# Kernel tuning notes

Measured on AMD Instinct MI355X. Metric: run time of the kernel, lower is better.

## Reference

```python
import jax, jax.numpy as jnp
import numpy as np

# Config matching init_kwargs: N=4 networks, dims 128 -> 1024 -> 1024 -> 512
A, B, D = 8, 2048, 128     # agents, batch, input size
N = 4                       # number of independent SePS networks
H1, H2, H3 = 1024, 1024, 512


def setup_inputs() -> dict:
    key = jax.random.key(0)
    ks = jax.random.split(key, 6)
    inputs = jax.random.normal(ks[0], (A, B, D), dtype=jnp.float32)  # stacked per-agent obs
    seps_indices = jax.random.randint(ks[1], (B, A), 0, N)           # cluster id per (sample, agent)
    scale = lambda k, shape, fan: jax.random.normal(k, shape, dtype=jnp.float32) * (1.0 / np.sqrt(fan))
    W0 = scale(ks[2], (N, D, H1), D);   b0 = jnp.zeros((N, H1), jnp.float32)
    W1 = scale(ks[3], (N, H1, H2), H1); b1 = jnp.zeros((N, H2), jnp.float32)
    W2 = scale(ks[4], (N, H2, H3), H2); b2 = jnp.zeros((N, H3), jnp.float32)
    return {"inputs": inputs, "seps_indices": seps_indices,
            "W0": W0, "b0": b0, "W1": W1, "b1": b1, "W2": W2, "b2": b2}


def reference(inputs, seps_indices, W0, b0, W1, b1, W2, b2):
    # Run every network densely on the full stacked input, as the torch module does.
    # inputs: [A, B, D]; W*: [N, in, out]
    h = jax.nn.relu(jnp.einsum('abd,ndh->nabh', inputs, W0) + b0[:, None, None, :])
    h = jax.nn.relu(jnp.einsum('nabh,nhk->nabk', h, W1) + b1[:, None, None, :])
    out_all = jnp.einsum('nabk,nko->nabo', h, W2) + b2[:, None, None, :]  # [N, A, B, H3]
    # Gather along the network axis per (agent, sample): seps_indices is [B, A]
    idx = seps_indices.T                              # [A, B]
    a = jnp.arange(inputs.shape[0])[:, None]          # [A, 1]
    b = jnp.arange(inputs.shape[1])[None, :]          # [1, B]
    return out_all[idx, a, b, :]                      # [A, B, H3] (stacked per-agent outputs)
```

## Files before the change

kernel.cpp:

```cpp
#include <hip/hip_runtime.h>
#include <hip/hip_bf16.h>

#define AG 8
#define BT 2048
#define RT (AG*BT)
#define NNET 4
#define D0 128
#define H1 1024
#define H2 1024
#define H3 512

typedef __attribute__((ext_vector_type(8))) short short8;
typedef __attribute__((ext_vector_type(4))) float f32x4;

__device__ __forceinline__ float bf2f(unsigned short u){
  return __uint_as_float(((unsigned int)u) << 16);
}
__device__ __forceinline__ unsigned short f2bf(float f){
  unsigned int x = __float_as_uint(f);
  x += 0x7fff + ((x >> 16) & 1);
  return (unsigned short)(x >> 16);
}

__device__ __forceinline__ void gload_lds16(const void* g, void* l){
  __builtin_amdgcn_global_load_lds(
      (const __attribute__((address_space(1))) unsigned int*)g,
      (__attribute__((address_space(3))) unsigned int*)l, 16, 0, 0);
}

__device__ __forceinline__ int bucket_off(const int* counts, int n){
  int s = 0;
  #pragma unroll
  for (int i = 0; i < NNET-1; i++) if (i < n) s += counts[i];
  return s;
}

__global__ void k_init(int* counts){
  if (threadIdx.x < NNET) counts[threadIdx.x] = 0;
}

__global__ __launch_bounds__(256) void k_compact(const int* __restrict__ seps,
                          int* __restrict__ counts, int* __restrict__ rowlist){
  __shared__ int lcount[NNET];
  __shared__ int lbase[NNET];
  int t = blockIdx.x * 256 + threadIdx.x;
  if (threadIdx.x < NNET) lcount[threadIdx.x] = 0;
  __syncthreads();
  int a = t >> 11, b = t & (BT-1);
  int n = seps[b*AG + a];
  int lrank = atomicAdd(&lcount[n], 1);
  __syncthreads();
  if (threadIdx.x < NNET)
    lbase[threadIdx.x] = atomicAdd(&counts[threadIdx.x], lcount[threadIdx.x]);
  __syncthreads();
  rowlist[n*RT + lbase[n] + lrank] = t;
}

template<int K, int NOUT>
__global__ __launch_bounds__(256) void k_transpose(const float* __restrict__ W,
                                                   unsigned short* __restrict__ WT){
  __shared__ float tile[32][33];
  int n = blockIdx.z;
  int k0 = blockIdx.x*32, o0 = blockIdx.y*32;
  const float* Wn = W + (size_t)n*K*NOUT;
  unsigned short* WTn = WT + (size_t)n*NOUT*K;
  int tx = threadIdx.x & 31, ty0 = threadIdx.x >> 5;
  #pragma unroll
  for (int r = 0; r < 32; r += 8)
    tile[ty0 + r][tx] = Wn[(size_t)(k0 + ty0 + r)*NOUT + o0 + tx];
  __syncthreads();
  #pragma unroll
  for (int r = 0; r < 32; r += 8)
    WTn[(size_t)(o0 + ty0 + r)*K + k0 + tx] = f2bf(tile[tx][ty0 + r]);
}

__global__ __launch_bounds__(256) void k_gather0(const float* __restrict__ X,
                          const int* __restrict__ counts,
                          const int* __restrict__ rowlist, unsigned short* __restrict__ X0h){
  int n = blockIdx.y;
  int cnt = counts[n];
  int i = blockIdx.x*16 + (threadIdx.x >> 4);
  if (i >= cnt) return;
  int off = bucket_off(counts, n);
  int orig = rowlist[n*RT + i];
  int c = (threadIdx.x & 15) * 8;
  const float* src = X + (size_t)orig*D0 + c;
  float4 v0 = *(const float4*)src, v1 = *(const float4*)(src+4);
  ushort4 u0, u1;
  u0.x=f2bf(v0.x); u0.y=f2bf(v0.y); u0.z=f2bf(v0.z); u0.w=f2bf(v0.w);
  u1.x=f2bf(v1.x); u1.y=f2bf(v1.y); u1.z=f2bf(v1.z); u1.w=f2bf(v1.w);
  unsigned short* dst = X0h + (size_t)(off + i)*D0 + c;
  *(ushort4*)dst = u0; *(ushort4*)(dst+4) = u1;
}

template<int K, int NOUT, int RELU, int SCATTER>
__global__ __launch_bounds__(256) void k_mlp(
    const unsigned short* __restrict__ X,
    const unsigned short* __restrict__ WT,
    const float* __restrict__ Bias,
    const int* __restrict__ counts,
    const int* __restrict__ rowlist,
    unsigned short* __restrict__ Yh,
    float* __restrict__ Yf)
{
  const int n = blockIdx.z;
  const int cnt = counts[n];
  const int i0 = blockIdx.x * 128;
  if (i0 >= cnt) return;
  const int off = bucket_off(counts, n);
  const int bn = blockIdx.y * 128;

  __shared__ __align__(16) unsigned short As[2][128*32];
  __shared__ __align__(16) unsigned short Bs[2][128*32];
  __shared__ int rs[128];

  const int t = threadIdx.x, lane = t & 63, wave = t >> 6;
  const int wm = wave >> 1, wn = wave & 1;
  const int lr = lane & 15, g = lane >> 4;

  if (SCATTER && t < 128) rs[t] = rowlist[n*RT + min(i0 + t, cnt-1)];

  const unsigned short* pA[2]; const unsigned short* pB[2];
  unsigned int ldsoff[2];
  const unsigned short* WTn = WT + (size_t)n * NOUT * K;
  #pragma unroll
  for (int j = 0; j < 2; j++){
    int r  = (j*4 + wave)*16 + (lane >> 2);
    int ps = lane & 3;
    int ls = ps ^ ((r >> 1) & 3);
    int rA = min(i0 + r, cnt-1);
    pA[j] = X   + (size_t)(off + rA)*K + ls*8;
    pB[j] = WTn + (size_t)(bn  + r )*K + ls*8;
    ldsoff[j] = (unsigned)(j*4 + wave) * 512;
  }

  int aoff[4], boff[4];
  #pragma unroll
  for (int i = 0; i < 4; i++){
    int ra = wm*64 + i*16 + lr;
    aoff[i] = ra*32 + (g ^ ((ra>>1)&3))*8;
    int rb = wn*64 + i*16 + lr;
    boff[i] = rb*32 + (g ^ ((rb>>1)&3))*8;
  }

  #pragma unroll
  for (int j = 0; j < 2; j++){
    gload_lds16(pA[j], &As[0][ldsoff[j]]);
    gload_lds16(pB[j], &Bs[0][ldsoff[j]]);
    pA[j] += 32; pB[j] += 32;
  }
  __syncthreads();

  f32x4 acc[4][4] = {};
  int cur = 0;
  for (int k0 = 0; k0 < K; k0 += 32){
    if (k0 + 32 < K){
      #pragma unroll
      for (int j = 0; j < 2; j++){
        gload_lds16(pA[j], &As[cur^1][ldsoff[j]]);
        gload_lds16(pB[j], &Bs[cur^1][ldsoff[j]]);
        pA[j] += 32; pB[j] += 32;
      }
    }
    short8 av[4], bv[4];
    #pragma unroll
    for (int i = 0; i < 4; i++) av[i] = *(const short8*)&As[cur][aoff[i]];
    #pragma unroll
    for (int i = 0; i < 4; i++) bv[i] = *(const short8*)&Bs[cur][boff[i]];
    __builtin_amdgcn_s_setprio(1);
    #pragma unroll
    for (int mi = 0; mi < 4; mi++)
      #pragma unroll
      for (int ni = 0; ni < 4; ni++)
        acc[mi][ni] = __builtin_amdgcn_mfma_f32_16x16x32_bf16(bv[ni], av[mi], acc[mi][ni], 0, 0, 0);
    __builtin_amdgcn_s_setprio(0);
    __syncthreads();
    cur ^= 1;
  }

  f32x4 bias4[4];
  #pragma unroll
  for (int ni = 0; ni < 4; ni++)
    bias4[ni] = *(const f32x4*)&Bias[n*NOUT + bn + wn*64 + ni*16 + g*4];

  #pragma unroll
  for (int mi = 0; mi < 4; mi++){
    int rloc = wm*64 + mi*16 + lr;
    int grow = i0 + rloc;
    if (grow < cnt){
      #pragma unroll
      for (int ni = 0; ni < 4; ni++){
        float o[4];
        #pragma unroll
        for (int i = 0; i < 4; i++){
          float v = acc[mi][ni][i] + bias4[ni][i];
          if (RELU) v = fmaxf(v, 0.f);
          o[i] = v;
        }
        int cb = bn + wn*64 + ni*16 + (g<<2);
        if (SCATTER){
          *(float4*)&Yf[(size_t)rs[rloc]*NOUT + cb] = make_float4(o[0],o[1],o[2],o[3]);
        } else {
          ushort4 u;
          u.x=f2bf(o[0]); u.y=f2bf(o[1]); u.z=f2bf(o[2]); u.w=f2bf(o[3]);
          *(ushort4*)&Yh[(size_t)(off + grow)*NOUT + cb] = u;
        }
      }
    }
  }
}

extern "C" void kernel_launch(void* const* d_in, const int* in_sizes, int n_in,
                              void* d_out, int out_size, void* d_ws, size_t ws_size,
                              hipStream_t stream) {
  const float* inputs = (const float*)d_in[0];
  const int*   seps   = (const int*)  d_in[1];
  const float* W0     = (const float*)d_in[2];
  const float* b0     = (const float*)d_in[3];
  const float* W1     = (const float*)d_in[4];
  const float* b1     = (const float*)d_in[5];
  const float* W2     = (const float*)d_in[6];
  const float* b2     = (const float*)d_in[7];
  float* out = (float*)d_out;

  char* ws = (char*)d_ws;
  int* counts  = (int*)ws;
  int* rowlist = (int*)(ws + 4096);
  const size_t MB = 1u << 20;
  unsigned short* WT0 = (unsigned short*)(ws + 1*MB);
  unsigned short* WT1 = (unsigned short*)(ws + 2*MB);
  unsigned short* WT2 = (unsigned short*)(ws + 10*MB);
  unsigned short* h1  = (unsigned short*)(ws + 14*MB);
  unsigned short* h2  = (unsigned short*)(ws + 46*MB);
  unsigned short* X0h = (unsigned short*)(ws + 46*MB);

  k_init   <<<1, 64, 0, stream>>>(counts);
  k_compact<<<RT/256, 256, 0, stream>>>(seps, counts, rowlist);

  k_transpose<D0, H1><<<dim3(D0/32, H1/32, NNET), 256, 0, stream>>>(W0, WT0);
  k_transpose<H1, H2><<<dim3(H1/32, H2/32, NNET), 256, 0, stream>>>(W1, WT1);
  k_transpose<H2, H3><<<dim3(H2/32, H3/32, NNET), 256, 0, stream>>>(W2, WT2);
  k_gather0<<<dim3(RT/16, NNET), 256, 0, stream>>>(inputs, counts, rowlist, X0h);

  k_mlp<D0, H1, 1, 0><<<dim3(RT/128, H1/128, NNET), 256, 0, stream>>>(
      X0h, WT0, b0, counts, rowlist, h1, nullptr);
  k_mlp<H1, H2, 1, 0><<<dim3(RT/128, H2/128, NNET), 256, 0, stream>>>(
      h1, WT1, b1, counts, rowlist, h2, nullptr);
  k_mlp<H2, H3, 0, 1><<<dim3(RT/128, H3/128, NNET), 256, 0, stream>>>(
      h2, WT2, b2, counts, rowlist, nullptr, out);
}
```

Before: 158.2 us.

## Use triple-buffered LDS pipeline with explicit vmcnt waits in MLP GEMM

Replaces the double-buffered global-to-LDS prefetch with a three-stage ring buffer and keeps two tiles in flight. Explicit s_waitcnt vmcnt counts and raw s_barriers replace the full __syncthreads, so that global loads overlap more with MFMA work. The reload of a stage is issued right after its fragments are read into registers. This raises LDS use per block, which may lower occupancy, and it depends on hand-counted vmcnt values being correct.

New measurement: 152.1 us. 3.9% less time.

```diff
diff --git a/kernel.cpp b/kernel.cpp
--- a/kernel.cpp
+++ b/kernel.cpp
@@ -12,6 +12,8 @@
 
 typedef __attribute__((ext_vector_type(8))) short short8;
 typedef __attribute__((ext_vector_type(4))) float f32x4;
+
+#define VMWAIT(N) asm volatile("s_waitcnt vmcnt(" #N ")" ::: "memory")
 
 __device__ __forceinline__ float bf2f(unsigned short u){
   return __uint_as_float(((unsigned int)u) << 16);
@@ -103,6 +105,7 @@
     unsigned short* __restrict__ Yh,
     float* __restrict__ Yf)
 {
+  constexpr int T = K / 32;
   const int n = blockIdx.z;
   const int cnt = counts[n];
   const int i0 = blockIdx.x * 128;
@@ -110,8 +113,8 @@
   const int off = bucket_off(counts, n);
   const int bn = blockIdx.y * 128;
 
-  __shared__ __align__(16) unsigned short As[2][128*32];
-  __shared__ __align__(16) unsigned short Bs[2][128*32];
+  __shared__ __align__(16) unsigned short As[3][128*32];
+  __shared__ __align__(16) unsigned short Bs[3][128*32];
   __shared__ int rs[128];
 
   const int t = threadIdx.x, lane = t & 63, wave = t >> 6;
@@ -143,30 +146,44 @@
     boff[i] = rb*32 + (g ^ ((rb>>1)&3))*8;
   }
 
-  #pragma unroll
-  for (int j = 0; j < 2; j++){
-    gload_lds16(pA[j], &As[0][ldsoff[j]]);
-    gload_lds16(pB[j], &Bs[0][ldsoff[j]]);
-    pA[j] += 32; pB[j] += 32;
-  }
-  __syncthreads();
+  __syncthreads();
+
+  #pragma unroll
+  for (int s = 0; s < 3; ++s){
+    #pragma unroll
+    for (int j = 0; j < 2; j++){
+      gload_lds16(pA[j], &As[s][ldsoff[j]]);
+      gload_lds16(pB[j], &Bs[s][ldsoff[j]]);
+      pA[j] += 32; pB[j] += 32;
+    }
+  }
 
   f32x4 acc[4][4] = {};
-  int cur = 0;
-  for (int k0 = 0; k0 < K; k0 += 32){
-    if (k0 + 32 < K){
+  int b = 0;
+  for (int ks = 0; ks < T; ++ks){
+    if (ks < T-2)       VMWAIT(8);
+    else if (ks == T-2) VMWAIT(4);
+    else                VMWAIT(0);
+    __builtin_amdgcn_s_barrier();
+
+    short8 av[4], bv[4];
+    #pragma unroll
+    for (int i = 0; i < 4; i++) av[i] = *(const short8*)&As[b][aoff[i]];
+    #pragma unroll
+    for (int i = 0; i < 4; i++) bv[i] = *(const short8*)&Bs[b][boff[i]];
+    asm volatile("s_waitcnt lgkmcnt(0)" ::: "memory");
+    __builtin_amdgcn_sched_barrier(0);
+    __builtin_amdgcn_s_barrier();
+
+    if (ks + 3 < T){
       #pragma unroll
       for (int j = 0; j < 2; j++){
-        gload_lds16(pA[j], &As[cur^1][ldsoff[j]]);
-        gload_lds16(pB[j], &Bs[cur^1][ldsoff[j]]);
+        gload_lds16(pA[j], &As[b][ldsoff[j]]);
+        gload_lds16(pB[j], &Bs[b][ldsoff[j]]);
         pA[j] += 32; pB[j] += 32;
       }
     }
-    short8 av[4], bv[4];
-    #pragma unroll
-    for (int i = 0; i < 4; i++) av[i] = *(const short8*)&As[cur][aoff[i]];
-    #pragma unroll
-    for (int i = 0; i < 4; i++) bv[i] = *(const short8*)&Bs[cur][boff[i]];
+
     __builtin_amdgcn_s_setprio(1);
     #pragma unroll
     for (int mi = 0; mi < 4; mi++)
@@ -174,8 +191,8 @@
       for (int ni = 0; ni < 4; ni++)
         acc[mi][ni] = __builtin_amdgcn_mfma_f32_16x16x32_bf16(bv[ni], av[mi], acc[mi][ni], 0, 0, 0);
     __builtin_amdgcn_s_setprio(0);
-    __syncthreads();
-    cur ^= 1;
+
+    b = (b == 2) ? 0 : b + 1;
   }
 
   f32x4 bias4[4];
```
